# Optimization experiments

Hardware: AMD Instinct MI355X
Metric: run time of the kernel (lower is better)

Reference implementation:

```python
import jax, jax.numpy as jnp
import numpy as np

DIM = 1024
H = 16
HKV = 4
HD = DIM // H  # 64
GROUP = H // HKV
ROPE_BASE = 10000.0
B, T = 2, 2048


def rms_norm(x, eps):
    return x * jax.lax.rsqrt(jnp.mean(x * x, axis=-1, keepdims=True) + eps)


def apply_rotary(x, cos, sin):
    # x: [B, h, T, HD]; cos/sin: [1, 1, T, HD//2]
    half = x.shape[-1] // 2
    x1, x2 = x[..., :half], x[..., half:]
    return jnp.concatenate([x1 * cos + x2 * sin, -x1 * sin + x2 * cos], axis=-1)


def setup_inputs() -> dict:
    key = jax.random.key(0)
    ks = jax.random.split(key, 5)
    s = 0.02
    return {
        "x": jax.random.normal(ks[0], (B, T, DIM), dtype=jnp.float32),
        "Wq": jax.random.normal(ks[1], (DIM, DIM), dtype=jnp.float32) * s,
        "Wk": jax.random.normal(ks[2], (HKV * HD, DIM), dtype=jnp.float32) * s,
        "Wv": jax.random.normal(ks[3], (HKV * HD, DIM), dtype=jnp.float32) * s,
        "Wproj": jax.random.normal(ks[4], (DIM, DIM), dtype=jnp.float32) * s,
        "q_gain": jnp.full((H,), 12.0, dtype=jnp.float32),
    }


def reference(x, Wq, Wk, Wv, Wproj, q_gain):
    bsz, seqlen, dim = x.shape
    eps = jnp.asarray(jnp.finfo(x.dtype).eps, x.dtype)

    # double RMSNorm path: normalized input for q/k, raw input for v
    x_qk = rms_norm(x, eps)
    q = (x_qk @ Wq.T).reshape(bsz, seqlen, H, HD).transpose(0, 2, 1, 3)    # [B,H,T,D]
    k = (x_qk @ Wk.T).reshape(bsz, seqlen, HKV, HD).transpose(0, 2, 1, 3)  # [B,Hkv,T,D]
    v = (x @ Wv.T).reshape(bsz, seqlen, HKV, HD).transpose(0, 2, 1, 3)     # [B,Hkv,T,D]

    q = rms_norm(q, eps)
    k = rms_norm(k, eps)

    # rotary embeddings
    t = jnp.arange(seqlen, dtype=jnp.float32)
    inv_freq = 1.0 / (ROPE_BASE ** (jnp.arange(0, HD, 2, dtype=jnp.float32) / HD))
    freqs = jnp.outer(t, inv_freq)                       # [T, HD//2]
    cos = jnp.cos(freqs)[None, None].astype(x.dtype)
    sin = jnp.sin(freqs)[None, None].astype(x.dtype)
    q = apply_rotary(q, cos, sin)
    k = apply_rotary(k, cos, sin)

    # per-head gain on q
    q = q * q_gain.astype(q.dtype)[None, :, None, None]

    # GQA: expand kv heads to query heads
    k_r = jnp.repeat(k, GROUP, axis=1)  # [B,H,T,D]
    v_r = jnp.repeat(v, GROUP, axis=1)

    scale = 1.0 / np.sqrt(HD)
    scores = jnp.einsum("bhqd,bhkd->bhqk", q, k_r) * scale
    causal = jnp.tril(jnp.ones((seqlen, seqlen), dtype=bool))
    scores = jnp.where(causal[None, None], scores, jnp.asarray(-jnp.inf, scores.dtype))
    attn = jax.nn.softmax(scores, axis=-1)
    y = jnp.einsum("bhqk,bhkd->bhqd", attn, v_r)          # [B,H,T,D]

    # XSA: remove value-direction component from output
    y_bt = y.transpose(0, 2, 1, 3)                        # [B,T,H,D]
    v_bt = v.transpose(0, 2, 1, 3)                        # [B,T,Hkv,D]
    y_g = y_bt.reshape(bsz, seqlen, HKV, GROUP, HD)
    vnorm = jnp.sqrt(jnp.sum(v_bt * v_bt, axis=-1, keepdims=True))
    vn = (v_bt / jnp.maximum(vnorm, 1e-12))[..., None, :]  # [B,T,Hkv,1,D]
    proj = jnp.sum(y_g * vn, axis=-1, keepdims=True) * vn
    y_bt = (y_g - proj).reshape(bsz, seqlen, H, HD)

    return y_bt.reshape(bsz, seqlen, dim) @ Wproj.T
```

## Files before the change

kernel.cpp:

```cpp
#include <hip/hip_runtime.h>
#include <hip/hip_bf16.h>

typedef __attribute__((ext_vector_type(8))) short bf8v;
typedef __attribute__((ext_vector_type(4))) float f4v;

#define MFMA16(a,b,c) __builtin_amdgcn_mfma_f32_16x16x32_bf16((a),(b),(c),0,0,0)

#define GLD16(gp, lp) __builtin_amdgcn_global_load_lds( \
    (const __attribute__((address_space(1))) void*)(gp), \
    (__attribute__((address_space(3))) void*)(lp), 16, 0, 0)

#define DIMC   1024
#define TSEQ   2048
#define NH     16
#define NKV    4
#define HDIM   64
#define RMS_EPS 1.1920929e-07f
#define QSCALE 0.1803368801111601f

__device__ __forceinline__ ushort f2bf(float f) {
  unsigned u = __builtin_bit_cast(unsigned, f);
  u = (u + 0x7FFFu + ((u >> 16) & 1u)) >> 16;
  return (ushort)u;
}
__device__ __forceinline__ float bf2f(ushort u) {
  return __builtin_bit_cast(float, (unsigned)u << 16);
}
__device__ __forceinline__ unsigned cvtpk(float lo, float hi) {
  unsigned r;
  asm("v_cvt_pk_bf16_f32 %0, %1, %2" : "=v"(r) : "v"(lo), "v"(hi));
  return r;
}

__global__ __launch_bounds__(256) void prep_w(
    const float* __restrict__ Wq, const float* __restrict__ Wk,
    const float* __restrict__ Wv, const float* __restrict__ Wp,
    ushort* __restrict__ wqkh, ushort* __restrict__ wqkl,
    ushort* __restrict__ wvb, ushort* __restrict__ wpb,
    float* __restrict__ cosT, float* __restrict__ sinT) {
  int bid = blockIdx.x, tid = threadIdx.x;
  if (bid < 1280) {
    const float* src;
    size_t si, di;
    if (bid < 1024) { src = Wq; si = (size_t)bid * 256 + tid; di = si; }
    else { src = Wk; si = (size_t)(bid - 1024) * 256 + tid; di = 262144 + si; }
    float4 v = ((const float4*)src)[si];
    ushort4 h, l;
    h.x = f2bf(v.x); l.x = f2bf(v.x - bf2f(h.x));
    h.y = f2bf(v.y); l.y = f2bf(v.y - bf2f(h.y));
    h.z = f2bf(v.z); l.z = f2bf(v.z - bf2f(h.z));
    h.w = f2bf(v.w); l.w = f2bf(v.w - bf2f(h.w));
    ((ushort4*)wqkh)[di] = h;
    ((ushort4*)wqkl)[di] = l;
  } else if (bid < 2560) {
    const float* src;
    ushort* dst;
    int i;
    if (bid < 1536) { src = Wv; dst = wvb; i = (bid - 1280) * 256 + tid; }
    else            { src = Wp; dst = wpb; i = (bid - 1536) * 256 + tid; }
    float4 v = ((const float4*)src)[i];
    ushort4 o;
    o.x = f2bf(v.x); o.y = f2bf(v.y); o.z = f2bf(v.z); o.w = f2bf(v.w);
    ((ushort4*)dst)[i] = o;
  } else {
    int i = (bid - 2560) * 256 + tid;
    int t = i >> 5, j = i & 31;
    float inv = 1.0f / powf(10000.0f, (float)j * (1.0f / 32.0f));
    float f = (float)t * inv;
    cosT[i] = cosf(f);
    sinT[i] = sinf(f);
  }
}

__global__ __launch_bounds__(256) void prep_x(const float* __restrict__ x,
                                              ushort* __restrict__ xhi,
                                              ushort* __restrict__ xlo,
                                              ushort* __restrict__ xb) {
  int row = blockIdx.x;
  int t = threadIdx.x;
  int lane = t & 63, w = t >> 6;
  float4 v = ((const float4*)(x + (size_t)row * DIMC))[t];
  float ss = v.x * v.x + v.y * v.y + v.z * v.z + v.w * v.w;
  for (int off = 32; off; off >>= 1) ss += __shfl_xor(ss, off);
  __shared__ float red[4];
  if (lane == 0) red[w] = ss;
  __syncthreads();
  float tot = red[0] + red[1] + red[2] + red[3];
  float rs = rsqrtf(tot * (1.0f / DIMC) + RMS_EPS);
  float n0 = v.x * rs, n1 = v.y * rs, n2 = v.z * rs, n3 = v.w * rs;
  ushort4 h, l, ob;
  h.x = f2bf(n0); l.x = f2bf(n0 - bf2f(h.x));
  h.y = f2bf(n1); l.y = f2bf(n1 - bf2f(h.y));
  h.z = f2bf(n2); l.z = f2bf(n2 - bf2f(h.z));
  h.w = f2bf(n3); l.w = f2bf(n3 - bf2f(h.w));
  ob.x = f2bf(v.x); ob.y = f2bf(v.y); ob.z = f2bf(v.z); ob.w = f2bf(v.w);
  ((ushort4*)(xhi + (size_t)row * DIMC))[t] = h;
  ((ushort4*)(xlo + (size_t)row * DIMC))[t] = l;
  ((ushort4*)(xb  + (size_t)row * DIMC))[t] = ob;
}

__global__ __launch_bounds__(256, 2)
void gemm_qkv(const ushort* __restrict__ xhi, const ushort* __restrict__ xlo,
              const ushort* __restrict__ wqkh, const ushort* __restrict__ wqkl,
              float* __restrict__ QKf, const ushort* __restrict__ xb,
              const ushort* __restrict__ wvb, float* __restrict__ Vf) {
  __shared__ __align__(16) ushort lA[128 * 64];
  __shared__ __align__(16) ushort lB[128 * 64];
  const int bx = blockIdx.x;
  const bool vpath = (bx >= 10);
  const ushort* A0 = vpath ? xb : xhi;
  const ushort* A1 = vpath ? xb : xlo;
  const ushort* B0 = vpath ? wvb : wqkh;
  const ushort* B1 = vpath ? wvb : wqkl;
  float* C = vpath ? Vf : QKf;
  const int N = vpath ? 256 : 1280;
  const int n0 = vpath ? (bx - 10) * 128 : bx * 128;
  const int nseg = vpath ? 1 : 3;

  const int t = threadIdx.x;
  const int lane = t & 63, w = t >> 6;
  const int wr = w >> 1, wc = w & 1;
  const int l15 = lane & 15, lg = lane >> 4;
  const int m0 = blockIdx.y * 128;
  const int srow = t >> 3, scp = t & 7;

  f4v acc[4][4] = {};

  for (int k0 = 0; k0 < nseg * 1024; k0 += 64) {
    const int seg = k0 >> 10, kk = k0 & 1023;
    const ushort* Ab = (seg == 1) ? A1 : A0;
    const ushort* Bb = (seg == 2) ? B1 : B0;
    for (int i = 0; i < 4; ++i) {
      int row = srow + i * 32;
      int sc = scp ^ (row & 7);
      const ushort* ga = Ab + (size_t)(m0 + row) * DIMC + kk + sc * 8;
      const ushort* gb = Bb + (size_t)(n0 + row) * DIMC + kk + sc * 8;
      GLD16(ga, &lA[w * 512 + i * 2048]);
      GLD16(gb, &lB[w * 512 + i * 2048]);
    }
    __syncthreads();
    for (int kx = 0; kx < 2; ++kx) {
      bf8v af[4], bfr[4];
      for (int m = 0; m < 4; ++m) {
        int row = wr * 64 + m * 16 + l15;
        int ch = (kx * 4 + lg) ^ (row & 7);
        af[m] = *(const bf8v*)&lA[row * 64 + ch * 8];
      }
      for (int n = 0; n < 4; ++n) {
        int row = wc * 64 + n * 16 + l15;
        int ch = (kx * 4 + lg) ^ (row & 7);
        bfr[n] = *(const bf8v*)&lB[row * 64 + ch * 8];
      }
      for (int m = 0; m < 4; ++m)
        for (int n = 0; n < 4; ++n)
          acc[m][n] = MFMA16(af[m], bfr[n], acc[m][n]);
    }
    __syncthreads();
  }

  for (int m = 0; m < 4; ++m)
    for (int n = 0; n < 4; ++n)
      for (int j = 0; j < 4; ++j) {
        int r = m0 + wr * 64 + m * 16 + lg * 4 + j;
        int c = n0 + wc * 64 + n * 16 + l15;
        C[(size_t)r * N + c] = acc[m][n][j];
      }
}

__global__ __launch_bounds__(256, 2)
void gemm_bt(const ushort* __restrict__ A0, const ushort* __restrict__ B0,
             float* __restrict__ C, int N) {
  __shared__ __align__(16) ushort lA[128 * 64];
  __shared__ __align__(16) ushort lB[128 * 64];
  const int t = threadIdx.x;
  const int lane = t & 63, w = t >> 6;
  const int wr = w >> 1, wc = w & 1;
  const int l15 = lane & 15, lg = lane >> 4;
  const int m0 = blockIdx.y * 128, n0 = blockIdx.x * 128;
  const int srow = t >> 3, scp = t & 7;

  f4v acc[4][4] = {};

  for (int k0 = 0; k0 < 1024; k0 += 64) {
    for (int i = 0; i < 4; ++i) {
      int row = srow + i * 32;
      int sc = scp ^ (row & 7);
      const ushort* ga = A0 + (size_t)(m0 + row) * DIMC + k0 + sc * 8;
      const ushort* gb = B0 + (size_t)(n0 + row) * DIMC + k0 + sc * 8;
      GLD16(ga, &lA[w * 512 + i * 2048]);
      GLD16(gb, &lB[w * 512 + i * 2048]);
    }
    __syncthreads();
    for (int kx = 0; kx < 2; ++kx) {
      bf8v af[4], bfr[4];
      for (int m = 0; m < 4; ++m) {
        int row = wr * 64 + m * 16 + l15;
        int ch = (kx * 4 + lg) ^ (row & 7);
        af[m] = *(const bf8v*)&lA[row * 64 + ch * 8];
      }
      for (int n = 0; n < 4; ++n) {
        int row = wc * 64 + n * 16 + l15;
        int ch = (kx * 4 + lg) ^ (row & 7);
        bfr[n] = *(const bf8v*)&lB[row * 64 + ch * 8];
      }
      for (int m = 0; m < 4; ++m)
        for (int n = 0; n < 4; ++n)
          acc[m][n] = MFMA16(af[m], bfr[n], acc[m][n]);
    }
    __syncthreads();
  }

  for (int m = 0; m < 4; ++m)
    for (int n = 0; n < 4; ++n)
      for (int j = 0; j < 4; ++j) {
        int r = m0 + wr * 64 + m * 16 + lg * 4 + j;
        int c = n0 + wc * 64 + n * 16 + l15;
        C[(size_t)r * N + c] = acc[m][n][j];
      }
}

__global__ __launch_bounds__(256) void qkv_post(
    const float* __restrict__ QKf, const float* __restrict__ cosT,
    const float* __restrict__ sinT, const float* __restrict__ qgain,
    ushort* __restrict__ qhi, ushort* __restrict__ qlo,
    ushort* __restrict__ kb16) {
  int m = blockIdx.x;
  int b = m >> 11, tpos = m & 2047;
  int lane = threadIdx.x & 63, w = threadIdx.x >> 6;
  int d = lane, j = d & 31;
  float sgn = (d < 32) ? 1.0f : -1.0f;
  float c = cosT[tpos * 32 + j], s = sinT[tpos * 32 + j];

  for (int i = 0; i < 4; ++i) {
    int h = w * 4 + i;
    float q = QKf[(size_t)m * 1280 + h * HDIM + d];
    float ss = q * q;
    for (int off = 32; off; off >>= 1) ss += __shfl_xor(ss, off);
    float rs = rsqrtf(ss * (1.0f / HDIM) + RMS_EPS);
    float qn = q * rs;
    float partner = __shfl_xor(qn, 32);
    float ro = (qn * c + sgn * partner * s) * (qgain[h] * QSCALE);
    ushort hi = f2bf(ro);
    ushort lo = f2bf(ro - bf2f(hi));
    size_t idx = (((size_t)b * NH + h) * TSEQ + tpos) * HDIM + d;
    qhi[idx] = hi;
    qlo[idx] = lo;
  }
  {
    int kv = w;
    float k = QKf[(size_t)m * 1280 + 1024 + kv * HDIM + d];
    float ss = k * k;
    for (int off = 32; off; off >>= 1) ss += __shfl_xor(ss, off);
    float rs = rsqrtf(ss * (1.0f / HDIM) + RMS_EPS);
    float kn = k * rs;
    float partner = __shfl_xor(kn, 32);
    float ro = kn * c + sgn * partner * s;
    kb16[((size_t)(b * NKV + kv) * TSEQ + tpos) * HDIM + d] = f2bf(ro);
  }
}

__global__ __launch_bounds__(256) void vtrans(const float* __restrict__ Vf,
                                              ushort* __restrict__ vt2,
                                              ushort* __restrict__ vhat_t) {
  __shared__ float lds[64][69];
  __shared__ float rnv[64];
  int bid = blockIdx.x;
  int bkv = bid >> 5, tt = bid & 31;
  int b = bkv >> 2, kv = bkv & 3;
  int tid = threadIdx.x;
  for (int i = 0; i < 16; ++i) {
    int idx = i * 256 + tid;
    int tloc = idx >> 6, d = idx & 63;
    lds[d][tloc] = Vf[((size_t)(b * TSEQ + tt * 64 + tloc)) * 256 + kv * 64 + d];
  }
  __syncthreads();
  {
    int t = tid >> 2, prt = tid & 3;
    float ssum = 0.f;
    for (int dd = 0; dd < 16; ++dd) {
      float v = lds[prt * 16 + dd][t];
      ssum += v * v;
    }
    ssum += __shfl_xor(ssum, 1);
    ssum += __shfl_xor(ssum, 2);
    if (prt == 0) rnv[t] = 1.0f / fmaxf(sqrtf(ssum), 1e-12f);
  }
  __syncthreads();
  for (int i = 0; i < 16; ++i) {
    int idx = i * 256 + tid;
    int d = idx >> 6, tloc = idx & 63;
    float v = lds[d][tloc];
    vt2[(size_t)bkv * (TSEQ * 64) + tt * 4096 + d * 64 + tloc] = f2bf(v);
    vhat_t[(size_t)bkv * (TSEQ * 64) + (size_t)d * TSEQ + tt * 64 + tloc] = f2bf(v * rnv[tloc]);
  }
}

__global__ __launch_bounds__(256, 4) void attn_kern(
    const ushort* __restrict__ qhi, const ushort* __restrict__ qlo,
    const ushort* __restrict__ kb16, const ushort* __restrict__ vt2,
    const ushort* __restrict__ vhat_t, ushort* __restrict__ ytil) {
  __shared__ __align__(16) ushort lk[2][64 * 64];
  __shared__ __align__(16) ushort lv[2][64 * 64];
  __shared__ __align__(16) unsigned pl[4][512];
  const int t = threadIdx.x;
  const int lane = t & 63, w = t >> 6;
  const int bid = blockIdx.x;
  const int xcd = bid & 7, g = (bid >> 3) & 3, trank = bid >> 5;
  const int tile = 31 - trank;
  const int b = xcd >> 2, kv = xcd & 3, h = kv * 4 + g;
  const int l15 = lane & 15, lg = lane >> 4;
  const int q0 = tile * 64 + w * 16;
  const int ntile = tile + 1;
  const int t3 = t >> 3, tc8 = t & 7;
  const int rx = l15 & 7;
  const int pswz = rx << 2;

  const size_t qoff = (((size_t)(b * NH + h)) * TSEQ + q0 + l15) * HDIM;
  bf8v bq0h = *(const bf8v*)(qhi + qoff + lg * 8);
  bf8v bq1h = *(const bf8v*)(qhi + qoff + 32 + lg * 8);
  bf8v bq0l = *(const bf8v*)(qlo + qoff + lg * 8);
  bf8v bq1l = *(const bf8v*)(qlo + qoff + 32 + lg * 8);

  const ushort* kb = kb16 + (size_t)(b * NKV + kv) * TSEQ * 64;
  const ushort* vb = vt2 + (size_t)(b * NKV + kv) * TSEQ * 64;
  unsigned* pw = &pl[w][0];

#define STAGE(BUF, IT) do { \
    _Pragma("unroll") \
    for (int i = 0; i < 2; ++i) { \
      int row = i * 32 + t3; \
      int sc = tc8 ^ (row & 7); \
      GLD16(kb + (size_t)((IT) * 64 + row) * 64 + sc * 8, \
            &lk[BUF][(i * 32 + (w << 3)) * 64]); \
      GLD16(vb + (size_t)(IT) * 4096 + row * 64 + sc * 8, \
            &lv[BUF][(i * 32 + (w << 3)) * 64]); \
    } } while (0)

  STAGE(0, 0);

  f4v y[4] = {};
  float mrow = -1e30f, lrow = 0.f;

#pragma unroll 1
  for (int it = 0; it < ntile; ++it) {
    const int cur = it & 1;
    __syncthreads();
    if (it + 1 < ntile) STAGE(cur ^ 1, it + 1);

    const ushort* lkc = &lk[cur][0];
    const ushort* lvc = &lv[cur][0];
    const int kv0 = it * 64;

    f4v s[4];
    __builtin_amdgcn_s_setprio(1);
#pragma unroll
    for (int n = 0; n < 4; ++n) {
      const ushort* krow = lkc + (n * 16 + l15) * 64;
      bf8v kh0 = *(const bf8v*)&krow[((0 + lg) ^ rx) * 8];
      bf8v kh1 = *(const bf8v*)&krow[((4 + lg) ^ rx) * 8];
      f4v z = {};
      f4v acc = MFMA16(kh0, bq0h, z);
      acc = MFMA16(kh1, bq1h, acc);
      acc = MFMA16(kh0, bq0l, acc);
      acc = MFMA16(kh1, bq1l, acc);
      s[n] = acc;
    }
    __builtin_amdgcn_s_setprio(0);

    const bool need_mask = (it == ntile - 1);
    float mloc = -1e30f;
#pragma unroll
    for (int n = 0; n < 4; ++n)
#pragma unroll
      for (int j = 0; j < 4; ++j) {
        float v = s[n][j];
        if (need_mask && (kv0 + n * 16 + lg * 4 + j > q0 + l15)) v = -1e30f;
        s[n][j] = v;
        mloc = fmaxf(mloc, v);
      }
    mloc = fmaxf(mloc, __shfl_xor(mloc, 16));
    mloc = fmaxf(mloc, __shfl_xor(mloc, 32));
    if (__any(mloc > mrow + 11.5f)) {
      float mnew = fmaxf(mrow, mloc);
      float scf = exp2f(mrow - mnew);
      lrow *= scf;
#pragma unroll
      for (int n = 0; n < 4; ++n) y[n] *= scf;
      mrow = mnew;
    }
    float rs = 0.f;
#pragma unroll
    for (int n = 0; n < 4; ++n)
#pragma unroll
      for (int j = 0; j < 4; ++j) {
        float e = exp2f(s[n][j] - mrow);
        s[n][j] = e;
        rs += e;
      }
    rs += __shfl_xor(rs, 16);
    rs += __shfl_xor(rs, 32);
    lrow += rs;

#pragma unroll
    for (int n = 0; n < 4; ++n) {
      uint2 pk;
      pk.x = cvtpk(s[n][0], s[n][1]);
      pk.y = cvtpk(s[n][2], s[n][3]);
      *(uint2*)&pw[l15 * 32 + ((8 * n + 2 * lg) ^ pswz)] = pk;
    }
    asm volatile("s_waitcnt lgkmcnt(0)" ::: "memory");
    bf8v pb0 = *(const bf8v*)&pw[l15 * 32 + ((lg * 4) ^ pswz)];
    bf8v pb1 = *(const bf8v*)&pw[l15 * 32 + ((16 + lg * 4) ^ pswz)];
    __builtin_amdgcn_s_setprio(1);
#pragma unroll
    for (int n = 0; n < 4; ++n) {
      const ushort* vrow = lvc + (n * 16 + l15) * 64;
      bf8v va0 = *(const bf8v*)&vrow[((0 + lg) ^ rx) * 8];
      bf8v va1 = *(const bf8v*)&vrow[((4 + lg) ^ rx) * 8];
      y[n] = MFMA16(va0, pb0, y[n]);
      y[n] = MFMA16(va1, pb1, y[n]);
    }
    __builtin_amdgcn_s_setprio(0);
  }
#undef STAGE

  {
    float inv = 1.0f / lrow;
    const ushort* vh = vhat_t + (size_t)(b * NKV + kv) * TSEQ * 64;
    ushort* yw = (ushort*)pw;
    float vv[4][4];
    float dp = 0.f;
#pragma unroll
    for (int n = 0; n < 4; ++n)
#pragma unroll
      for (int j = 0; j < 4; ++j) {
        int d = n * 16 + lg * 4 + j;
        float yv = y[n][j] * inv;
        y[n][j] = yv;
        vv[n][j] = bf2f(vh[(size_t)d * TSEQ + q0 + l15]);
        dp += yv * vv[n][j];
      }
    dp += __shfl_xor(dp, 16);
    dp += __shfl_xor(dp, 32);
#pragma unroll
    for (int n = 0; n < 4; ++n)
#pragma unroll
      for (int j = 0; j < 4; ++j) {
        int d = n * 16 + lg * 4 + j;
        yw[l15 * 64 + (((d >> 3) ^ rx) << 3) + (d & 7)] = f2bf(y[n][j] - dp * vv[n][j]);
      }
    asm volatile("s_waitcnt lgkmcnt(0)" ::: "memory");
    int row = lane >> 2, quad = lane & 3;
    bf8v y0 = *(const bf8v*)(yw + row * 64 + ((quad ^ (row & 7)) << 3));
    bf8v y1 = *(const bf8v*)(yw + row * 64 + (((quad + 4) ^ (row & 7)) << 3));
    size_t gbase = ((size_t)(b * TSEQ + q0 + row)) * DIMC + h * HDIM + quad * 8;
    *(bf8v*)(ytil + gbase) = y0;
    *(bf8v*)(ytil + gbase + 32) = y1;
  }
}

extern "C" void kernel_launch(void* const* d_in, const int* in_sizes, int n_in,
                              void* d_out, int out_size, void* d_ws, size_t ws_size,
                              hipStream_t stream) {
  (void)in_sizes; (void)n_in; (void)out_size; (void)ws_size;
  const float* x  = (const float*)d_in[0];
  const float* Wq = (const float*)d_in[1];
  const float* Wk = (const float*)d_in[2];
  const float* Wv = (const float*)d_in[3];
  const float* Wp = (const float*)d_in[4];
  const float* qg = (const float*)d_in[5];
  float* out = (float*)d_out;
  char* ws = (char*)d_ws;
  const size_t KB = 1024, MB = 1ull << 20;

  ushort* xhi = (ushort*)(ws);
  ushort* xlo = (ushort*)(ws + 8 * MB);
  ushort* xb  = (ushort*)(ws + 16 * MB);
  ushort* wqkh = (ushort*)(ws + 24 * MB);
  ushort* wqkl = (ushort*)(ws + 26 * MB + 512 * KB);
  ushort* wvb = (ushort*)(ws + 29 * MB);
  ushort* wpb = (ushort*)(ws + 29 * MB + 512 * KB);
  float*  cosT = (float*)(ws + 31 * MB + 512 * KB);
  float*  sinT = (float*)(ws + 31 * MB + 768 * KB);
  float*  QKf  = (float*)(ws + 32 * MB);
  ushort* kb16 = (ushort*)(ws + 52 * MB);
  ushort* vt2  = (ushort*)(ws + 54 * MB);
  ushort* vhat = (ushort*)(ws + 56 * MB);

  float*  Vf   = out;
  ushort* qhb  = xhi;
  ushort* qlb  = xlo;
  ushort* ytil = xb;

  prep_w<<<2816, 256, 0, stream>>>(Wq, Wk, Wv, Wp, wqkh, wqkl, wvb, wpb,
                                   cosT, sinT);
  prep_x<<<4096, 256, 0, stream>>>(x, xhi, xlo, xb);

  gemm_qkv<<<dim3(12, 32), 256, 0, stream>>>(xhi, xlo, wqkh, wqkl, QKf,
                                             xb, wvb, Vf);

  qkv_post<<<4096, 256, 0, stream>>>(QKf, cosT, sinT, qg, qhb, qlb, kb16);
  vtrans<<<256, 256, 0, stream>>>(Vf, vt2, vhat);
  attn_kern<<<1024, 256, 0, stream>>>(qhb, qlb, kb16, vt2, vhat, ytil);
  gemm_bt<<<dim3(8, 32), 256, 0, stream>>>(ytil, wpb, out, 1024);
}
```

Baseline: 160.8 us.

## Merge prep and post kernels, reorder causal attention tile schedule

```diff
diff --git a/kernel.cpp b/kernel.cpp
--- a/kernel.cpp
+++ b/kernel.cpp
@@ -32,18 +32,45 @@
   return r;
 }
 
-__global__ __launch_bounds__(256) void prep_w(
+__global__ __launch_bounds__(256) void prep_all(
+    const float* __restrict__ x,
     const float* __restrict__ Wq, const float* __restrict__ Wk,
     const float* __restrict__ Wv, const float* __restrict__ Wp,
+    ushort* __restrict__ xhi, ushort* __restrict__ xlo,
+    ushort* __restrict__ xb,
     ushort* __restrict__ wqkh, ushort* __restrict__ wqkl,
     ushort* __restrict__ wvb, ushort* __restrict__ wpb,
     float* __restrict__ cosT, float* __restrict__ sinT) {
+  __shared__ float red[4];
   int bid = blockIdx.x, tid = threadIdx.x;
-  if (bid < 1280) {
+  if (bid < 4096) {
+    int row = bid;
+    int lane = tid & 63, w = tid >> 6;
+    float4 v = ((const float4*)(x + (size_t)row * DIMC))[tid];
+    float ss = v.x * v.x + v.y * v.y + v.z * v.z + v.w * v.w;
+    for (int off = 32; off; off >>= 1) ss += __shfl_xor(ss, off);
+    if (lane == 0) red[w] = ss;
+    __syncthreads();
+    float tot = red[0] + red[1] + red[2] + red[3];
+    float rs = rsqrtf(tot * (1.0f / DIMC) + RMS_EPS);
+    float n0 = v.x * rs, n1 = v.y * rs, n2 = v.z * rs, n3 = v.w * rs;
+    ushort4 h, l, ob;
+    h.x = f2bf(n0); l.x = f2bf(n0 - bf2f(h.x));
+    h.y = f2bf(n1); l.y = f2bf(n1 - bf2f(h.y));
+    h.z = f2bf(n2); l.z = f2bf(n2 - bf2f(h.z));
+    h.w = f2bf(n3); l.w = f2bf(n3 - bf2f(h.w));
+    ob.x = f2bf(v.x); ob.y = f2bf(v.y); ob.z = f2bf(v.z); ob.w = f2bf(v.w);
+    ((ushort4*)(xhi + (size_t)row * DIMC))[tid] = h;
+    ((ushort4*)(xlo + (size_t)row * DIMC))[tid] = l;
+    ((ushort4*)(xb  + (size_t)row * DIMC))[tid] = ob;
+    return;
+  }
+  int wb = bid - 4096;
+  if (wb < 1280) {
     const float* src;
     size_t si, di;
-    if (bid < 1024) { src = Wq; si = (size_t)bid * 256 + tid; di = si; }
-    else { src = Wk; si = (size_t)(bid - 1024) * 256 + tid; di = 262144 + si; }
+    if (wb < 1024) { src = Wq; si = (size_t)wb * 256 + tid; di = si; }
+    else { src = Wk; si = (size_t)(wb - 1024) * 256 + tid; di = 262144 + si; }
     float4 v = ((const float4*)src)[si];
     ushort4 h, l;
     h.x = f2bf(v.x); l.x = f2bf(v.x - bf2f(h.x));
@@ -52,51 +79,24 @@
     h.w = f2bf(v.w); l.w = f2bf(v.w - bf2f(h.w));
     ((ushort4*)wqkh)[di] = h;
     ((ushort4*)wqkl)[di] = l;
-  } else if (bid < 2560) {
+  } else if (wb < 2560) {
     const float* src;
     ushort* dst;
     int i;
-    if (bid < 1536) { src = Wv; dst = wvb; i = (bid - 1280) * 256 + tid; }
-    else            { src = Wp; dst = wpb; i = (bid - 1536) * 256 + tid; }
+    if (wb < 1536) { src = Wv; dst = wvb; i = (wb - 1280) * 256 + tid; }
+    else           { src = Wp; dst = wpb; i = (wb - 1536) * 256 + tid; }
     float4 v = ((const float4*)src)[i];
     ushort4 o;
     o.x = f2bf(v.x); o.y = f2bf(v.y); o.z = f2bf(v.z); o.w = f2bf(v.w);
     ((ushort4*)dst)[i] = o;
   } else {
-    int i = (bid - 2560) * 256 + tid;
+    int i = (wb - 2560) * 256 + tid;
     int t = i >> 5, j = i & 31;
     float inv = 1.0f / powf(10000.0f, (float)j * (1.0f / 32.0f));
     float f = (float)t * inv;
     cosT[i] = cosf(f);
     sinT[i] = sinf(f);
   }
-}
-
-__global__ __launch_bounds__(256) void prep_x(const float* __restrict__ x,
-                                              ushort* __restrict__ xhi,
-                                              ushort* __restrict__ xlo,
-                                              ushort* __restrict__ xb) {
-  int row = blockIdx.x;
-  int t = threadIdx.x;
-  int lane = t & 63, w = t >> 6;
-  float4 v = ((const float4*)(x + (size_t)row * DIMC))[t];
-  float ss = v.x * v.x + v.y * v.y + v.z * v.z + v.w * v.w;
-  for (int off = 32; off; off >>= 1) ss += __shfl_xor(ss, off);
-  __shared__ float red[4];
-  if (lane == 0) red[w] = ss;
-  __syncthreads();
-  float tot = red[0] + red[1] + red[2] + red[3];
-  float rs = rsqrtf(tot * (1.0f / DIMC) + RMS_EPS);
-  float n0 = v.x * rs, n1 = v.y * rs, n2 = v.z * rs, n3 = v.w * rs;
-  ushort4 h, l, ob;
-  h.x = f2bf(n0); l.x = f2bf(n0 - bf2f(h.x));
-  h.y = f2bf(n1); l.y = f2bf(n1 - bf2f(h.y));
-  h.z = f2bf(n2); l.z = f2bf(n2 - bf2f(h.z));
-  h.w = f2bf(n3); l.w = f2bf(n3 - bf2f(h.w));
-  ob.x = f2bf(v.x); ob.y = f2bf(v.y); ob.z = f2bf(v.z); ob.w = f2bf(v.w);
-  ((ushort4*)(xhi + (size_t)row * DIMC))[t] = h;
-  ((ushort4*)(xlo + (size_t)row * DIMC))[t] = l;
-  ((ushort4*)(xb  + (size_t)row * DIMC))[t] = ob;
 }
 
 __global__ __launch_bounds__(256, 2)
@@ -219,79 +219,82 @@
       }
 }
 
-__global__ __launch_bounds__(256) void qkv_post(
+__global__ __launch_bounds__(256) void post_all(
     const float* __restrict__ QKf, const float* __restrict__ cosT,
     const float* __restrict__ sinT, const float* __restrict__ qgain,
     ushort* __restrict__ qhi, ushort* __restrict__ qlo,
-    ushort* __restrict__ kb16) {
-  int m = blockIdx.x;
-  int b = m >> 11, tpos = m & 2047;
-  int lane = threadIdx.x & 63, w = threadIdx.x >> 6;
-  int d = lane, j = d & 31;
-  float sgn = (d < 32) ? 1.0f : -1.0f;
-  float c = cosT[tpos * 32 + j], s = sinT[tpos * 32 + j];
-
-  for (int i = 0; i < 4; ++i) {
-    int h = w * 4 + i;
-    float q = QKf[(size_t)m * 1280 + h * HDIM + d];
-    float ss = q * q;
-    for (int off = 32; off; off >>= 1) ss += __shfl_xor(ss, off);
-    float rs = rsqrtf(ss * (1.0f / HDIM) + RMS_EPS);
-    float qn = q * rs;
-    float partner = __shfl_xor(qn, 32);
-    float ro = (qn * c + sgn * partner * s) * (qgain[h] * QSCALE);
-    ushort hi = f2bf(ro);
-    ushort lo = f2bf(ro - bf2f(hi));
-    size_t idx = (((size_t)b * NH + h) * TSEQ + tpos) * HDIM + d;
-    qhi[idx] = hi;
-    qlo[idx] = lo;
-  }
-  {
-    int kv = w;
-    float k = QKf[(size_t)m * 1280 + 1024 + kv * HDIM + d];
-    float ss = k * k;
-    for (int off = 32; off; off >>= 1) ss += __shfl_xor(ss, off);
-    float rs = rsqrtf(ss * (1.0f / HDIM) + RMS_EPS);
-    float kn = k * rs;
-    float partner = __shfl_xor(kn, 32);
-    float ro = kn * c + sgn * partner * s;
-    kb16[((size_t)(b * NKV + kv) * TSEQ + tpos) * HDIM + d] = f2bf(ro);
-  }
-}
-
-__global__ __launch_bounds__(256) void vtrans(const float* __restrict__ Vf,
-                                              ushort* __restrict__ vt2,
-                                              ushort* __restrict__ vhat_t) {
+    ushort* __restrict__ kb16,
+    const float* __restrict__ Vf, ushort* __restrict__ vt2,
+    ushort* __restrict__ vhat_t) {
   __shared__ float lds[64][69];
   __shared__ float rnv[64];
   int bid = blockIdx.x;
-  int bkv = bid >> 5, tt = bid & 31;
-  int b = bkv >> 2, kv = bkv & 3;
-  int tid = threadIdx.x;
-  for (int i = 0; i < 16; ++i) {
-    int idx = i * 256 + tid;
-    int tloc = idx >> 6, d = idx & 63;
-    lds[d][tloc] = Vf[((size_t)(b * TSEQ + tt * 64 + tloc)) * 256 + kv * 64 + d];
-  }
-  __syncthreads();
+  if (bid < 4096) {
+    int m = bid;
+    int b = m >> 11, tpos = m & 2047;
+    int lane = threadIdx.x & 63, w = threadIdx.x >> 6;
+    int d = lane, j = d & 31;
+    float sgn = (d < 32) ? 1.0f : -1.0f;
+    float c = cosT[tpos * 32 + j], s = sinT[tpos * 32 + j];
+
+    for (int i = 0; i < 4; ++i) {
+      int h = w * 4 + i;
+      float q = QKf[(size_t)m * 1280 + h * HDIM + d];
+      float ss = q * q;
+      for (int off = 32; off; off >>= 1) ss += __shfl_xor(ss, off);
+      float rs = rsqrtf(ss * (1.0f / HDIM) + RMS_EPS);
+      float qn = q * rs;
+      float partner = __shfl_xor(qn, 32);
+      float ro = (qn * c + sgn * partner * s) * (qgain[h] * QSCALE);
+      ushort hi = f2bf(ro);
+      ushort lo = f2bf(ro - bf2f(hi));
+      size_t idx = (((size_t)b * NH + h) * TSEQ + tpos) * HDIM + d;
+      qhi[idx] = hi;
+      qlo[idx] = lo;
+    }
+    {
+      int kv = w;
+      float k = QKf[(size_t)m * 1280 + 1024 + kv * HDIM + d];
+      float ss = k * k;
+      for (int off = 32; off; off >>= 1) ss += __shfl_xor(ss, off);
+      float rs = rsqrtf(ss * (1.0f / HDIM) + RMS_EPS);
+      float kn = k * rs;
+      float partner = __shfl_xor(kn, 32);
+      float ro = kn * c + sgn * partner * s;
+      kb16[((size_t)(b * NKV + kv) * TSEQ + tpos) * HDIM + d] = f2bf(ro);
+    }
+    return;
+  }
   {
-    int t = tid >> 2, prt = tid & 3;
-    float ssum = 0.f;
-    for (int dd = 0; dd < 16; ++dd) {
-      float v = lds[prt * 16 + dd][t];
-      ssum += v * v;
-    }
-    ssum += __shfl_xor(ssum, 1);
-    ssum += __shfl_xor(ssum, 2);
-    if (prt == 0) rnv[t] = 1.0f / fmaxf(sqrtf(ssum), 1e-12f);
-  }
-  __syncthreads();
-  for (int i = 0; i < 16; ++i) {
-    int idx = i * 256 + tid;
-    int d = idx >> 6, tloc = idx & 63;
-    float v = lds[d][tloc];
-    vt2[(size_t)bkv * (TSEQ * 64) + tt * 4096 + d * 64 + tloc] = f2bf(v);
-    vhat_t[(size_t)bkv * (TSEQ * 64) + (size_t)d * TSEQ + tt * 64 + tloc] = f2bf(v * rnv[tloc]);
+    int vb = bid - 4096;
+    int bkv = vb >> 5, tt = vb & 31;
+    int b = bkv >> 2, kv = bkv & 3;
+    int tid = threadIdx.x;
+    for (int i = 0; i < 16; ++i) {
+      int idx = i * 256 + tid;
+      int tloc = idx >> 6, d = idx & 63;
+      lds[d][tloc] = Vf[((size_t)(b * TSEQ + tt * 64 + tloc)) * 256 + kv * 64 + d];
+    }
+    __syncthreads();
+    {
+      int t = tid >> 2, prt = tid & 3;
+      float ssum = 0.f;
+      for (int dd = 0; dd < 16; ++dd) {
+        float v = lds[prt * 16 + dd][t];
+        ssum += v * v;
+      }
+      ssum += __shfl_xor(ssum, 1);
+      ssum += __shfl_xor(ssum, 2);
+      if (prt == 0) rnv[t] = 1.0f / fmaxf(sqrtf(ssum), 1e-12f);
+    }
+    __syncthreads();
+    for (int i = 0; i < 16; ++i) {
+      int idx = i * 256 + tid;
+      int d = idx >> 6, tloc = idx & 63;
+      float v = lds[d][tloc];
+      vt2[(size_t)bkv * (TSEQ * 64) + tt * 4096 + d * 64 + tloc] = f2bf(v);
+      vhat_t[(size_t)bkv * (TSEQ * 64) + (size_t)d * TSEQ + tt * 64 + tloc] = f2bf(v * rnv[tloc]);
+    }
   }
 }
 
@@ -306,7 +309,11 @@
   const int lane = t & 63, w = t >> 6;
   const int bid = blockIdx.x;
   const int xcd = bid & 7, g = (bid >> 3) & 3, trank = bid >> 5;
-  const int tile = 31 - trank;
+  const int ta = trank & 7, tq = trank >> 3;
+  const int tile = (tq == 0) ? (31 - ta)
+                 : (tq == 1) ? ta
+                 : (tq == 2) ? (23 - ta)
+                             : (8 + ta);
   const int b = xcd >> 2, kv = xcd & 3, h = kv * 4 + g;
   const int l15 = lane & 15, lg = lane >> 4;
   const int q0 = tile * 64 + w * 16;
@@ -492,15 +499,14 @@
   ushort* qlb  = xlo;
   ushort* ytil = xb;
 
-  prep_w<<<2816, 256, 0, stream>>>(Wq, Wk, Wv, Wp, wqkh, wqkl, wvb, wpb,
-                                   cosT, sinT);
-  prep_x<<<4096, 256, 0, stream>>>(x, xhi, xlo, xb);
+  prep_all<<<6912, 256, 0, stream>>>(x, Wq, Wk, Wv, Wp, xhi, xlo, xb,
+                                     wqkh, wqkl, wvb, wpb, cosT, sinT);
 
   gemm_qkv<<<dim3(12, 32), 256, 0, stream>>>(xhi, xlo, wqkh, wqkl, QKf,
                                              xb, wvb, Vf);
 
-  qkv_post<<<4096, 256, 0, stream>>>(QKf, cosT, sinT, qg, qhb, qlb, kb16);
-  vtrans<<<256, 256, 0, stream>>>(Vf, vt2, vhat);
+  post_all<<<4352, 256, 0, stream>>>(QKf, cosT, sinT, qg, qhb, qlb, kb16,
+                                     Vf, vt2, vhat);
   attn_kern<<<1024, 256, 0, stream>>>(qhb, qlb, kb16, vt2, vhat, ytil);
   gemm_bt<<<dim3(8, 32), 256, 0, stream>>>(ytil, wpb, out, 1024);
 }
```

New measurement: 153.7 us. -4.4%, faster.
